# Optimization experiments

Hardware: AMD Instinct MI355X
Metric: run time of the kernel (lower is better)

The kernel has to match this reference:

```python
import jax, jax.numpy as jnp
import numpy as np

BS, N, D_IN, HID, D_OUT = 16, 256, 128, 128, 128


def setup_inputs() -> dict:
    key = jax.random.key(0)
    ks = jax.random.split(key, 10)
    s = 0.02
    return {
        "x": jax.random.normal(ks[0], (BS, N, D_IN), dtype=jnp.float32),
        "adj": jax.random.randint(ks[1], (BS, N, N), 0, 2, dtype=jnp.int32),
        "W_fc": jax.random.normal(ks[2], (D_IN, HID), dtype=jnp.float32) * s,
        "b_fc": jnp.zeros((HID,), dtype=jnp.float32),
        "W_a1": jax.random.normal(ks[3], (2 * HID, HID), dtype=jnp.float32) * s,
        "b_a1": jnp.zeros((HID,), dtype=jnp.float32),
        "w_a2": jax.random.normal(ks[4], (HID,), dtype=jnp.float32) * s,
        "b_a2": jnp.zeros((), dtype=jnp.float32),
        "W_out": jax.random.normal(ks[5], (HID, D_OUT), dtype=jnp.float32) * s,
        "b_out": jnp.zeros((D_OUT,), dtype=jnp.float32),
    }


def reference(x, adj, W_fc, b_fc, W_a1, b_a1, w_a2, b_a2, W_out, b_out):
    # h = fc(x): (bs, n, hid)
    h = jnp.einsum("bnd,dh->bnh", x, W_fc) + b_fc
    # attn first layer on concat([h_i, h_j]) decomposes into two half-projections
    # (same math as Linear(2*hid, hid) on the concatenated pair features).
    a_i = jnp.einsum("bnh,hk->bnk", h, W_a1[:HID])  # contribution of h_i
    a_j = jnp.einsum("bnh,hk->bnk", h, W_a1[HID:])  # contribution of h_j
    pre = a_i[:, :, None, :] + a_j[:, None, :, :] + b_a1  # (bs, n, n, hid)
    e = jnp.einsum("bijk,k->bij", jax.nn.relu(pre), w_a2) + b_a2  # (bs, n, n)
    e = jnp.where(adj == 0, jnp.float32(-1e9), e)
    attn = jax.nn.softmax(e, axis=-1)
    h_prime = jnp.einsum("bij,bjh->bih", attn, h)
    out = jnp.einsum("bih,ho->bio", h_prime, W_out) + b_out
    return out
```

## Files before the change

kernel.cpp:

```cpp
#include <hip/hip_runtime.h>

#define BS  16
#define NN  256
#define HID 128

__device__ __forceinline__ int xcd_swz(int bid) {
    return (bid & 7) * 64 + (bid >> 3);
}

__global__ __launch_bounds__(512, 4) void gat_k1(
    const float* __restrict__ x, const float* __restrict__ W_fc,
    const float* __restrict__ b_fc, const float* __restrict__ W_a1,
    const float* __restrict__ b_a1, const float* __restrict__ W_out,
    float* __restrict__ aiT, float* __restrict__ ajT, float* __restrict__ g)
{
    __shared__ __align__(16) float xs[8][HID];
    __shared__ __align__(16) float hs[8][HID];
    __shared__ __align__(16) float red[4][8][HID];

    const int tid = threadIdx.x;
    const int k   = tid & 127;
    const int q   = tid >> 7;
    const int swz = xcd_swz(blockIdx.x);
    const int r0  = swz * 8;
    const int b   = r0 >> 8;
    const int n0  = r0 & 255;

    for (int t = tid; t < 8 * HID; t += 512)
        xs[t >> 7][t & 127] = x[r0 * HID + t];
    __syncthreads();

    {
        float acc[8] = {0,0,0,0,0,0,0,0};
        const int dq = 32 * q;
        #pragma unroll 2
        for (int d = 0; d < 32; d += 4) {
            float w[4];
            #pragma unroll
            for (int t = 0; t < 4; ++t) w[t] = W_fc[(dq + d + t) * HID + k];
            #pragma unroll
            for (int r = 0; r < 8; ++r) {
                const float4 xv = *(const float4*)&xs[r][dq + d];
                acc[r] += xv.x * w[0] + xv.y * w[1] + xv.z * w[2] + xv.w * w[3];
            }
        }
        #pragma unroll
        for (int r = 0; r < 8; ++r) red[q][r][k] = acc[r];
    }
    __syncthreads();

    {
        const float bf = b_fc[k];
        #pragma unroll
        for (int r2 = 0; r2 < 2; ++r2) {
            const int r = 2 * q + r2;
            hs[r][k] = (red[0][r][k] + red[1][r][k])
                     + (red[2][r][k] + red[3][r][k]) + bf;
        }
    }
    __syncthreads();

    {
        const int is_aj = q >> 1;
        const int half  = q & 1;
        const float* Wp = W_a1 + (is_aj * HID + half * 64) * HID;
        float acc[8] = {0,0,0,0,0,0,0,0};
        const int hb = half * 64;
        #pragma unroll 2
        for (int d = 0; d < 64; d += 4) {
            float w[4];
            #pragma unroll
            for (int t = 0; t < 4; ++t) w[t] = Wp[(d + t) * HID + k];
            #pragma unroll
            for (int r = 0; r < 8; ++r) {
                const float4 hv = *(const float4*)&hs[r][hb + d];
                acc[r] += hv.x * w[0] + hv.y * w[1] + hv.z * w[2] + hv.w * w[3];
            }
        }
        #pragma unroll
        for (int r = 0; r < 8; ++r) red[q][r][k] = acc[r];
    }
    __syncthreads();

    {
        const int is_aj = q >> 1;
        const int rb4   = (q & 1) * 4;
        const float bias = is_aj ? 0.f : b_a1[k];
        const int p0 = 2 * is_aj, p1 = 2 * is_aj + 1;
        float4 v;
        v.x = red[p0][rb4 + 0][k] + red[p1][rb4 + 0][k] + bias;
        v.y = red[p0][rb4 + 1][k] + red[p1][rb4 + 1][k] + bias;
        v.z = red[p0][rb4 + 2][k] + red[p1][rb4 + 2][k] + bias;
        v.w = red[p0][rb4 + 3][k] + red[p1][rb4 + 3][k] + bias;
        float* dst = (is_aj ? ajT : aiT) + (b * HID + k) * NN + n0 + rb4;
        *(float4*)dst = v;
    }
    __syncthreads();

    {
        float acc[8] = {0,0,0,0,0,0,0,0};
        const int dq = 32 * q;
        #pragma unroll 2
        for (int d = 0; d < 32; d += 4) {
            float w[4];
            #pragma unroll
            for (int t = 0; t < 4; ++t) w[t] = W_out[(dq + d + t) * HID + k];
            #pragma unroll
            for (int r = 0; r < 8; ++r) {
                const float4 hv = *(const float4*)&hs[r][dq + d];
                acc[r] += hv.x * w[0] + hv.y * w[1] + hv.z * w[2] + hv.w * w[3];
            }
        }
        #pragma unroll
        for (int r = 0; r < 8; ++r) red[q][r][k] = acc[r];
    }
    __syncthreads();

    {
        #pragma unroll
        for (int r2 = 0; r2 < 2; ++r2) {
            const int r = 2 * q + r2;
            g[(r0 + r) * HID + k] = (red[0][r][k] + red[1][r][k])
                                  + (red[2][r][k] + red[3][r][k]);
        }
    }
}

__global__ __launch_bounds__(512, 4) void gat_k2(
    const float* __restrict__ aiT, const float* __restrict__ ajT,
    const float* __restrict__ g,  const int* __restrict__ adj,
    const float* __restrict__ w_a2, const float* __restrict__ b_a2,
    const float* __restrict__ b_out, float* __restrict__ out)
{
    __shared__ __align__(16) float aiw[HID][8];
    __shared__ __align__(16) float w2s[HID];
    __shared__ __align__(16) float ep[8][NN];
    __shared__ __align__(16) float red[4][8][HID];

    const int tid = threadIdx.x;
    const int swz = xcd_swz(blockIdx.x);
    const int b   = swz >> 5;
    const int i0  = (swz & 31) * 8;
    const int wv  = tid >> 6, lane = tid & 63;

    for (int t = tid; t < HID * 8; t += 512) {
        const int kk = t >> 3, r = t & 7;
        aiw[kk][r] = aiT[(b * HID + kk) * NN + i0 + r];
    }
    if (tid < HID) w2s[tid] = w_a2[tid];
    __syncthreads();

    const int jj = 32 * wv + (lane & 31);
    const int rg = lane >> 5;
    {
        int am[4];
        #pragma unroll
        for (int r = 0; r < 4; ++r)
            am[r] = adj[(b * NN + i0 + 4 * rg + r) * NN + jj];

        const float* ajp = ajT + b * HID * NN + jj;
        float acc[4] = {0.f, 0.f, 0.f, 0.f};
        #pragma unroll 8
        for (int kk = 0; kk < HID; ++kk) {
            const float a   = ajp[kk * NN];
            const float4 f4 = *(const float4*)&aiw[kk][4 * rg];
            const float wk  = w2s[kk];
            acc[0] += fmaxf(f4.x + a, 0.f) * wk;
            acc[1] += fmaxf(f4.y + a, 0.f) * wk;
            acc[2] += fmaxf(f4.z + a, 0.f) * wk;
            acc[3] += fmaxf(f4.w + a, 0.f) * wk;
        }
        const float ba2 = b_a2[0];
        #pragma unroll
        for (int r = 0; r < 4; ++r)
            ep[4 * rg + r][jj] = am[r] ? acc[r] + ba2 : -1e9f;
    }
    __syncthreads();

    {
        float4 e4 = *(const float4*)&ep[wv][4 * lane];
        float m = fmaxf(fmaxf(e4.x, e4.y), fmaxf(e4.z, e4.w));
        #pragma unroll
        for (int off = 32; off; off >>= 1) m = fmaxf(m, __shfl_xor(m, off));
        const float p0 = __expf(e4.x - m), p1 = __expf(e4.y - m);
        const float p2 = __expf(e4.z - m), p3 = __expf(e4.w - m);
        float s = (p0 + p1) + (p2 + p3);
        #pragma unroll
        for (int off = 32; off; off >>= 1) s += __shfl_xor(s, off);
        const float inv = 1.f / s;
        const float4 pv = {p0 * inv, p1 * inv, p2 * inv, p3 * inv};
        *(float4*)&ep[wv][4 * lane] = pv;
    }
    __syncthreads();

    const int k = tid & 127, qh = tid >> 7;
    {
        float o[8] = {0,0,0,0,0,0,0,0};
        const float* gb = g + (b * NN + qh * 64) * HID + k;
        const int jb = qh * 64;
        #pragma unroll 2
        for (int jq = 0; jq < 64; jq += 4) {
            const float g0 = gb[(jq + 0) * HID];
            const float g1 = gb[(jq + 1) * HID];
            const float g2 = gb[(jq + 2) * HID];
            const float g3 = gb[(jq + 3) * HID];
            #pragma unroll
            for (int r = 0; r < 8; ++r) {
                const float4 pv = *(const float4*)&ep[r][jb + jq];
                o[r] += pv.x * g0 + pv.y * g1 + pv.z * g2 + pv.w * g3;
            }
        }
        #pragma unroll
        for (int r = 0; r < 8; ++r) red[qh][r][k] = o[r];
    }
    __syncthreads();

    {
        const float bo = b_out[k];
        #pragma unroll
        for (int r2 = 0; r2 < 2; ++r2) {
            const int r = 2 * qh + r2;
            out[(b * NN + i0 + r) * HID + k] =
                (red[0][r][k] + red[1][r][k]) +
                (red[2][r][k] + red[3][r][k]) + bo;
        }
    }
}

extern "C" void kernel_launch(void* const* d_in, const int* in_sizes, int n_in,
                              void* d_out, int out_size, void* d_ws, size_t ws_size,
                              hipStream_t stream) {
    const float* x     = (const float*)d_in[0];
    const int*   adj   = (const int*)  d_in[1];
    const float* W_fc  = (const float*)d_in[2];
    const float* b_fc  = (const float*)d_in[3];
    const float* W_a1  = (const float*)d_in[4];
    const float* b_a1  = (const float*)d_in[5];
    const float* w_a2  = (const float*)d_in[6];
    const float* b_a2  = (const float*)d_in[7];
    const float* W_out = (const float*)d_in[8];
    const float* b_out = (const float*)d_in[9];
    float* out = (float*)d_out;

    float* ws  = (float*)d_ws;
    float* aiT = ws;
    float* ajT = ws + BS * NN * HID;
    float* g   = ws + 2 * BS * NN * HID;

    gat_k1<<<BS * NN / 8, 512, 0, stream>>>(x, W_fc, b_fc, W_a1, b_a1, W_out,
                                            aiT, ajT, g);
    gat_k2<<<BS * (NN / 8), 512, 0, stream>>>(aiT, ajT, g, adj, w_a2, b_a2,
                                              b_out, out);
}
```

Before: 41.41 us.

## Restructure attention score loop with split-K, register prefetch and uniform ai loads

The attention-score stage of the second kernel is reorganised. Each wave now handles 8 query rows by 64 key columns over half of the hidden dimension, instead of 4 rows by 32 columns over all of it. The ai values are read as wave-uniform float8 loads straight from global memory rather than staged through LDS. The aj values are double-buffered in registers, 16 at a time. The two hidden-dimension halves are summed through a shared buffer during softmax, the adjacency read becomes one int4 per lane, and several GEMM loops in both kernels are unrolled further. The aim is more independent work per thread and fewer LDS round trips, at the cost of higher register pressure and an extra partial-sum reduction.

```diff
diff --git a/kernel.cpp b/kernel.cpp
--- a/kernel.cpp
+++ b/kernel.cpp
@@ -3,6 +3,8 @@
 #define BS  16
 #define NN  256
 #define HID 128
+
+typedef __attribute__((ext_vector_type(8))) float float8;
 
 __device__ __forceinline__ int xcd_swz(int bid) {
     return (bid & 7) * 64 + (bid >> 3);
@@ -33,7 +35,7 @@
     {
         float acc[8] = {0,0,0,0,0,0,0,0};
         const int dq = 32 * q;
-        #pragma unroll 2
+        #pragma unroll 4
         for (int d = 0; d < 32; d += 4) {
             float w[4];
             #pragma unroll
@@ -66,7 +68,7 @@
         const float* Wp = W_a1 + (is_aj * HID + half * 64) * HID;
         float acc[8] = {0,0,0,0,0,0,0,0};
         const int hb = half * 64;
-        #pragma unroll 2
+        #pragma unroll 4
         for (int d = 0; d < 64; d += 4) {
             float w[4];
             #pragma unroll
@@ -100,7 +102,7 @@
     {
         float acc[8] = {0,0,0,0,0,0,0,0};
         const int dq = 32 * q;
-        #pragma unroll 2
+        #pragma unroll 4
         for (int d = 0; d < 32; d += 4) {
             float w[4];
             #pragma unroll
@@ -132,10 +134,8 @@
     const float* __restrict__ w_a2, const float* __restrict__ b_a2,
     const float* __restrict__ b_out, float* __restrict__ out)
 {
-    __shared__ __align__(16) float aiw[HID][8];
-    __shared__ __align__(16) float w2s[HID];
-    __shared__ __align__(16) float ep[8][NN];
-    __shared__ __align__(16) float red[4][8][HID];
+    __shared__ __align__(16) float buf[2 * 8 * NN];
+    __shared__ __align__(16) float ep[8 * NN];
 
     const int tid = threadIdx.x;
     const int swz = xcd_swz(blockIdx.x);
@@ -143,53 +143,79 @@
     const int i0  = (swz & 31) * 8;
     const int wv  = tid >> 6, lane = tid & 63;
 
-    for (int t = tid; t < HID * 8; t += 512) {
-        const int kk = t >> 3, r = t & 7;
-        aiw[kk][r] = aiT[(b * HID + kk) * NN + i0 + r];
-    }
-    if (tid < HID) w2s[tid] = w_a2[tid];
-    __syncthreads();
-
-    const int jj = 32 * wv + (lane & 31);
-    const int rg = lane >> 5;
-    {
-        int am[4];
-        #pragma unroll
-        for (int r = 0; r < 4; ++r)
-            am[r] = adj[(b * NN + i0 + 4 * rg + r) * NN + jj];
-
-        const float* ajp = ajT + b * HID * NN + jj;
-        float acc[4] = {0.f, 0.f, 0.f, 0.f};
-        #pragma unroll 8
-        for (int kk = 0; kk < HID; ++kk) {
-            const float a   = ajp[kk * NN];
-            const float4 f4 = *(const float4*)&aiw[kk][4 * rg];
-            const float wk  = w2s[kk];
-            acc[0] += fmaxf(f4.x + a, 0.f) * wk;
-            acc[1] += fmaxf(f4.y + a, 0.f) * wk;
-            acc[2] += fmaxf(f4.z + a, 0.f) * wk;
-            acc[3] += fmaxf(f4.w + a, 0.f) * wk;
-        }
+    const int4 am = *(const int4*)(adj + (b * NN + i0 + wv) * NN + 4 * lane);
+
+    const int kh = wv >> 2, jq = wv & 3;
+    const int j  = jq * 64 + lane;
+    {
+        const float* ajp = ajT + (b * HID + kh * 64) * NN + j;
+        const int aoff = __builtin_amdgcn_readfirstlane((b * HID + kh * 64) * NN + i0);
+        const float* aip = aiT + aoff;
+        const float* w2p = w_a2 + kh * 64;
+
+        float acc[8] = {0,0,0,0,0,0,0,0};
+        float pa[16], pb[16];
+        #pragma unroll
+        for (int t = 0; t < 16; ++t) pa[t] = ajp[t * NN];
+        #pragma unroll
+        for (int t = 0; t < 16; ++t) pb[t] = ajp[(16 + t) * NN];
+
+        #pragma unroll
+        for (int c = 0; c < 64; c += 32) {
+            #pragma unroll
+            for (int t = 0; t < 16; ++t) {
+                const int kk = c + t;
+                const float8 s8 = *(const float8*)(aip + kk * NN);
+                const float wk  = w2p[kk];
+                const float a   = pa[t];
+                #pragma unroll
+                for (int r = 0; r < 8; ++r)
+                    acc[r] += fmaxf(s8[r] + a, 0.f) * wk;
+            }
+            if (c + 32 < 64) {
+                #pragma unroll
+                for (int t = 0; t < 16; ++t) pa[t] = ajp[(c + 32 + t) * NN];
+            }
+            #pragma unroll
+            for (int t = 0; t < 16; ++t) {
+                const int kk = c + 16 + t;
+                const float8 s8 = *(const float8*)(aip + kk * NN);
+                const float wk  = w2p[kk];
+                const float a   = pb[t];
+                #pragma unroll
+                for (int r = 0; r < 8; ++r)
+                    acc[r] += fmaxf(s8[r] + a, 0.f) * wk;
+            }
+            if (c + 48 < 64) {
+                #pragma unroll
+                for (int t = 0; t < 16; ++t) pb[t] = ajp[(c + 48 + t) * NN];
+            }
+        }
+        #pragma unroll
+        for (int r = 0; r < 8; ++r)
+            buf[(kh * 8 + r) * NN + j] = acc[r];
+    }
+    __syncthreads();
+
+    {
         const float ba2 = b_a2[0];
-        #pragma unroll
-        for (int r = 0; r < 4; ++r)
-            ep[4 * rg + r][jj] = am[r] ? acc[r] + ba2 : -1e9f;
-    }
-    __syncthreads();
-
-    {
-        float4 e4 = *(const float4*)&ep[wv][4 * lane];
-        float m = fmaxf(fmaxf(e4.x, e4.y), fmaxf(e4.z, e4.w));
+        const float4 u = *(const float4*)&buf[(0 + wv) * NN + 4 * lane];
+        const float4 v = *(const float4*)&buf[(8 + wv) * NN + 4 * lane];
+        const float e0 = am.x ? u.x + v.x + ba2 : -1e9f;
+        const float e1 = am.y ? u.y + v.y + ba2 : -1e9f;
+        const float e2 = am.z ? u.z + v.z + ba2 : -1e9f;
+        const float e3 = am.w ? u.w + v.w + ba2 : -1e9f;
+        float m = fmaxf(fmaxf(e0, e1), fmaxf(e2, e3));
         #pragma unroll
         for (int off = 32; off; off >>= 1) m = fmaxf(m, __shfl_xor(m, off));
-        const float p0 = __expf(e4.x - m), p1 = __expf(e4.y - m);
-        const float p2 = __expf(e4.z - m), p3 = __expf(e4.w - m);
+        const float p0 = __expf(e0 - m), p1 = __expf(e1 - m);
+        const float p2 = __expf(e2 - m), p3 = __expf(e3 - m);
         float s = (p0 + p1) + (p2 + p3);
         #pragma unroll
         for (int off = 32; off; off >>= 1) s += __shfl_xor(s, off);
         const float inv = 1.f / s;
         const float4 pv = {p0 * inv, p1 * inv, p2 * inv, p3 * inv};
-        *(float4*)&ep[wv][4 * lane] = pv;
+        *(float4*)&ep[wv * NN + 4 * lane] = pv;
     }
     __syncthreads();
 
@@ -198,20 +224,20 @@
         float o[8] = {0,0,0,0,0,0,0,0};
         const float* gb = g + (b * NN + qh * 64) * HID + k;
         const int jb = qh * 64;
-        #pragma unroll 2
-        for (int jq = 0; jq < 64; jq += 4) {
-            const float g0 = gb[(jq + 0) * HID];
-            const float g1 = gb[(jq + 1) * HID];
-            const float g2 = gb[(jq + 2) * HID];
-            const float g3 = gb[(jq + 3) * HID];
-            #pragma unroll
-            for (int r = 0; r < 8; ++r) {
-                const float4 pv = *(const float4*)&ep[r][jb + jq];
+        #pragma unroll 4
+        for (int jq2 = 0; jq2 < 64; jq2 += 4) {
+            const float g0 = gb[(jq2 + 0) * HID];
+            const float g1 = gb[(jq2 + 1) * HID];
+            const float g2 = gb[(jq2 + 2) * HID];
+            const float g3 = gb[(jq2 + 3) * HID];
+            #pragma unroll
+            for (int r = 0; r < 8; ++r) {
+                const float4 pv = *(const float4*)&ep[r * NN + jb + jq2];
                 o[r] += pv.x * g0 + pv.y * g1 + pv.z * g2 + pv.w * g3;
             }
         }
         #pragma unroll
-        for (int r = 0; r < 8; ++r) red[qh][r][k] = o[r];
+        for (int r = 0; r < 8; ++r) buf[(qh * 8 + r) * HID + k] = o[r];
     }
     __syncthreads();
 
@@ -221,8 +247,8 @@
         for (int r2 = 0; r2 < 2; ++r2) {
             const int r = 2 * qh + r2;
             out[(b * NN + i0 + r) * HID + k] =
-                (red[0][r][k] + red[1][r][k]) +
-                (red[2][r][k] + red[3][r][k]) + bo;
+                (buf[(0 + r) * HID + k]  + buf[(8 + r) * HID + k]) +
+                (buf[(16 + r) * HID + k] + buf[(24 + r) * HID + k]) + bo;
         }
     }
 }
```

Measured after the change: 44.08 us. 1.06x slower.

## Restructure attention score loop with relu identity and split-K across waves

Applied to the files above, without the earlier changes.

The edge-score loop in the second kernel uses relu(a+b) = max(a,-b) + b, which lets the a_j*w term sit in a shared accumulator while each term becomes a max and an FMA. Each wave now handles half of the hidden dimension and two rows over four columns per lane, using float4 loads of ajT. Partial sums go through a shared buffer and are combined in the softmax step, which also loads adj as int4. This aims to cut per-element ALU work and improve load vectorization, at the cost of an extra shared-memory reduction and sync, with the buffer reused as the later reduction scratch.

```diff
diff --git a/kernel.cpp b/kernel.cpp
--- a/kernel.cpp
+++ b/kernel.cpp
@@ -134,8 +134,8 @@
 {
     __shared__ __align__(16) float aiw[HID][8];
     __shared__ __align__(16) float w2s[HID];
+    __shared__ __align__(16) float buf[2][8][NN];
     __shared__ __align__(16) float ep[8][NN];
-    __shared__ __align__(16) float red[4][8][HID];
 
     const int tid = threadIdx.x;
     const int swz = xcd_swz(blockIdx.x);
@@ -148,42 +148,55 @@
         aiw[kk][r] = aiT[(b * HID + kk) * NN + i0 + r];
     }
     if (tid < HID) w2s[tid] = w_a2[tid];
-    __syncthreads();
-
-    const int jj = 32 * wv + (lane & 31);
-    const int rg = lane >> 5;
-    {
-        int am[4];
-        #pragma unroll
-        for (int r = 0; r < 4; ++r)
-            am[r] = adj[(b * NN + i0 + 4 * rg + r) * NN + jj];
-
-        const float* ajp = ajT + b * HID * NN + jj;
-        float acc[4] = {0.f, 0.f, 0.f, 0.f};
+
+    const int4 am = *(const int4*)(adj + (b * NN + i0 + wv) * NN + 4 * lane);
+    __syncthreads();
+
+    const int kh = wv >> 2, rp = wv & 3;
+    {
+        const float* ajp = ajT + (b * HID + kh * 64) * NN + 4 * lane;
+        float4 acc0 = {0,0,0,0}, acc1 = {0,0,0,0}, saw = {0,0,0,0};
+        const int kb = kh * 64;
         #pragma unroll 8
-        for (int kk = 0; kk < HID; ++kk) {
-            const float a   = ajp[kk * NN];
-            const float4 f4 = *(const float4*)&aiw[kk][4 * rg];
-            const float wk  = w2s[kk];
-            acc[0] += fmaxf(f4.x + a, 0.f) * wk;
-            acc[1] += fmaxf(f4.y + a, 0.f) * wk;
-            acc[2] += fmaxf(f4.z + a, 0.f) * wk;
-            acc[3] += fmaxf(f4.w + a, 0.f) * wk;
-        }
+        for (int t = 0; t < 64; ++t) {
+            const float4 a4 = *(const float4*)(ajp + t * NN);
+            const float2 f2 = *(const float2*)&aiw[kb + t][2 * rp];
+            const float wk  = w2s[kb + t];
+            saw.x  = __builtin_fmaf(a4.x, wk, saw.x);
+            saw.y  = __builtin_fmaf(a4.y, wk, saw.y);
+            saw.z  = __builtin_fmaf(a4.z, wk, saw.z);
+            saw.w  = __builtin_fmaf(a4.w, wk, saw.w);
+            acc0.x = __builtin_fmaf(fmaxf(f2.x, -a4.x), wk, acc0.x);
+            acc0.y = __builtin_fmaf(fmaxf(f2.x, -a4.y), wk, acc0.y);
+            acc0.z = __builtin_fmaf(fmaxf(f2.x, -a4.z), wk, acc0.z);
+            acc0.w = __builtin_fmaf(fmaxf(f2.x, -a4.w), wk, acc0.w);
+            acc1.x = __builtin_fmaf(fmaxf(f2.y, -a4.x), wk, acc1.x);
+            acc1.y = __builtin_fmaf(fmaxf(f2.y, -a4.y), wk, acc1.y);
+            acc1.z = __builtin_fmaf(fmaxf(f2.y, -a4.z), wk, acc1.z);
+            acc1.w = __builtin_fmaf(fmaxf(f2.y, -a4.w), wk, acc1.w);
+        }
+        const float4 e0 = {acc0.x + saw.x, acc0.y + saw.y,
+                           acc0.z + saw.z, acc0.w + saw.w};
+        const float4 e1 = {acc1.x + saw.x, acc1.y + saw.y,
+                           acc1.z + saw.z, acc1.w + saw.w};
+        *(float4*)&buf[kh][2 * rp + 0][4 * lane] = e0;
+        *(float4*)&buf[kh][2 * rp + 1][4 * lane] = e1;
+    }
+    __syncthreads();
+
+    {
         const float ba2 = b_a2[0];
-        #pragma unroll
-        for (int r = 0; r < 4; ++r)
-            ep[4 * rg + r][jj] = am[r] ? acc[r] + ba2 : -1e9f;
-    }
-    __syncthreads();
-
-    {
-        float4 e4 = *(const float4*)&ep[wv][4 * lane];
-        float m = fmaxf(fmaxf(e4.x, e4.y), fmaxf(e4.z, e4.w));
+        const float4 u = *(const float4*)&buf[0][wv][4 * lane];
+        const float4 v = *(const float4*)&buf[1][wv][4 * lane];
+        const float e0 = am.x ? u.x + v.x + ba2 : -1e9f;
+        const float e1 = am.y ? u.y + v.y + ba2 : -1e9f;
+        const float e2 = am.z ? u.z + v.z + ba2 : -1e9f;
+        const float e3 = am.w ? u.w + v.w + ba2 : -1e9f;
+        float m = fmaxf(fmaxf(e0, e1), fmaxf(e2, e3));
         #pragma unroll
         for (int off = 32; off; off >>= 1) m = fmaxf(m, __shfl_xor(m, off));
-        const float p0 = __expf(e4.x - m), p1 = __expf(e4.y - m);
-        const float p2 = __expf(e4.z - m), p3 = __expf(e4.w - m);
+        const float p0 = __expf(e0 - m), p1 = __expf(e1 - m);
+        const float p2 = __expf(e2 - m), p3 = __expf(e3 - m);
         float s = (p0 + p1) + (p2 + p3);
         #pragma unroll
         for (int off = 32; off; off >>= 1) s += __shfl_xor(s, off);
@@ -193,6 +206,7 @@
     }
     __syncthreads();
 
+    float* red = &buf[0][0][0];
     const int k = tid & 127, qh = tid >> 7;
     {
         float o[8] = {0,0,0,0,0,0,0,0};
@@ -211,7 +225,7 @@
             }
         }
         #pragma unroll
-        for (int r = 0; r < 8; ++r) red[qh][r][k] = o[r];
+        for (int r = 0; r < 8; ++r) red[(qh * 8 + r) * HID + k] = o[r];
     }
     __syncthreads();
 
@@ -221,8 +235,8 @@
         for (int r2 = 0; r2 < 2; ++r2) {
             const int r = 2 * qh + r2;
             out[(b * NN + i0 + r) * HID + k] =
-                (red[0][r][k] + red[1][r][k]) +
-                (red[2][r][k] + red[3][r][k]) + bo;
+                (red[(0 + r) * HID + k]  + red[(8 + r) * HID + k]) +
+                (red[(16 + r) * HID + k] + red[(24 + r) * HID + k]) + bo;
         }
     }
 }
```

Result: no change. 41.54 us (+0.3%).

## Rewrite GAT attention-score loop with relu identity and split-K waves, enlarge fc tile

Applied to the files above, without the earlier changes.

The attention-score kernel now uses relu(a+b) = max(a,-b) + b. The per-j term sum(aj*w) is accumulated once per column instead of per row pair. Each wave handles a quarter of the hidden dimension over half the columns, for all 8 rows, and the partial sums are reduced through shared memory. Adjacency is loaded as int4, and the final attn@g stage splits j across waves with float2 loads and an 8-way shared reduction. The projection kernel processes 16 rows per block instead of 8, which halves the grid to 256 blocks to reuse weight loads but raises register and LDS use per block.

```diff
diff --git a/kernel.cpp b/kernel.cpp
--- a/kernel.cpp
+++ b/kernel.cpp
@@ -4,7 +4,10 @@
 #define NN  256
 #define HID 128
 
-__device__ __forceinline__ int xcd_swz(int bid) {
+__device__ __forceinline__ int xcd_swz256(int bid) {
+    return (bid & 7) * 32 + (bid >> 3);
+}
+__device__ __forceinline__ int xcd_swz512(int bid) {
     return (bid & 7) * 64 + (bid >> 3);
 }
 
@@ -14,24 +17,26 @@
     const float* __restrict__ b_a1, const float* __restrict__ W_out,
     float* __restrict__ aiT, float* __restrict__ ajT, float* __restrict__ g)
 {
-    __shared__ __align__(16) float xs[8][HID];
-    __shared__ __align__(16) float hs[8][HID];
-    __shared__ __align__(16) float red[4][8][HID];
+    __shared__ __align__(16) float xs[16][HID];
+    __shared__ __align__(16) float hs[16][HID];
+    __shared__ __align__(16) float red[4][16][HID];
 
     const int tid = threadIdx.x;
     const int k   = tid & 127;
     const int q   = tid >> 7;
-    const int swz = xcd_swz(blockIdx.x);
-    const int r0  = swz * 8;
+    const int swz = xcd_swz256(blockIdx.x);
+    const int r0  = swz * 16;
     const int b   = r0 >> 8;
     const int n0  = r0 & 255;
 
-    for (int t = tid; t < 8 * HID; t += 512)
+    for (int t = tid; t < 16 * HID; t += 512)
         xs[t >> 7][t & 127] = x[r0 * HID + t];
     __syncthreads();
 
     {
-        float acc[8] = {0,0,0,0,0,0,0,0};
+        float acc[16];
+        #pragma unroll
+        for (int r = 0; r < 16; ++r) acc[r] = 0.f;
         const int dq = 32 * q;
         #pragma unroll 2
         for (int d = 0; d < 32; d += 4) {
@@ -39,21 +44,21 @@
             #pragma unroll
             for (int t = 0; t < 4; ++t) w[t] = W_fc[(dq + d + t) * HID + k];
             #pragma unroll
-            for (int r = 0; r < 8; ++r) {
+            for (int r = 0; r < 16; ++r) {
                 const float4 xv = *(const float4*)&xs[r][dq + d];
                 acc[r] += xv.x * w[0] + xv.y * w[1] + xv.z * w[2] + xv.w * w[3];
             }
         }
         #pragma unroll
-        for (int r = 0; r < 8; ++r) red[q][r][k] = acc[r];
+        for (int r = 0; r < 16; ++r) red[q][r][k] = acc[r];
     }
     __syncthreads();
 
     {
         const float bf = b_fc[k];
         #pragma unroll
-        for (int r2 = 0; r2 < 2; ++r2) {
-            const int r = 2 * q + r2;
+        for (int r2 = 0; r2 < 4; ++r2) {
+            const int r = 4 * q + r2;
             hs[r][k] = (red[0][r][k] + red[1][r][k])
                      + (red[2][r][k] + red[3][r][k]) + bf;
         }
@@ -64,7 +69,9 @@
         const int is_aj = q >> 1;
         const int half  = q & 1;
         const float* Wp = W_a1 + (is_aj * HID + half * 64) * HID;
-        float acc[8] = {0,0,0,0,0,0,0,0};
+        float acc[16];
+        #pragma unroll
+        for (int r = 0; r < 16; ++r) acc[r] = 0.f;
         const int hb = half * 64;
         #pragma unroll 2
         for (int d = 0; d < 64; d += 4) {
@@ -72,33 +79,35 @@
             #pragma unroll
             for (int t = 0; t < 4; ++t) w[t] = Wp[(d + t) * HID + k];
             #pragma unroll
-            for (int r = 0; r < 8; ++r) {
+            for (int r = 0; r < 16; ++r) {
                 const float4 hv = *(const float4*)&hs[r][hb + d];
                 acc[r] += hv.x * w[0] + hv.y * w[1] + hv.z * w[2] + hv.w * w[3];
             }
         }
         #pragma unroll
-        for (int r = 0; r < 8; ++r) red[q][r][k] = acc[r];
+        for (int r = 0; r < 16; ++r) red[q][r][k] = acc[r];
     }
     __syncthreads();
 
     {
         const int is_aj = q >> 1;
-        const int rb4   = (q & 1) * 4;
+        const int rb8   = (q & 1) * 8;
         const float bias = is_aj ? 0.f : b_a1[k];
         const int p0 = 2 * is_aj, p1 = 2 * is_aj + 1;
-        float4 v;
-        v.x = red[p0][rb4 + 0][k] + red[p1][rb4 + 0][k] + bias;
-        v.y = red[p0][rb4 + 1][k] + red[p1][rb4 + 1][k] + bias;
-        v.z = red[p0][rb4 + 2][k] + red[p1][rb4 + 2][k] + bias;
-        v.w = red[p0][rb4 + 3][k] + red[p1][rb4 + 3][k] + bias;
-        float* dst = (is_aj ? ajT : aiT) + (b * HID + k) * NN + n0 + rb4;
-        *(float4*)dst = v;
-    }
-    __syncthreads();
-
-    {
-        float acc[8] = {0,0,0,0,0,0,0,0};
+        float v[8];
+        #pragma unroll
+        for (int t = 0; t < 8; ++t)
+            v[t] = red[p0][rb8 + t][k] + red[p1][rb8 + t][k] + bias;
+        float* dst = (is_aj ? ajT : aiT) + (b * HID + k) * NN + n0 + rb8;
+        *(float4*)(dst + 0) = *(float4*)&v[0];
+        *(float4*)(dst + 4) = *(float4*)&v[4];
+    }
+    __syncthreads();
+
+    {
+        float acc[16];
+        #pragma unroll
+        for (int r = 0; r < 16; ++r) acc[r] = 0.f;
         const int dq = 32 * q;
         #pragma unroll 2
         for (int d = 0; d < 32; d += 4) {
@@ -106,20 +115,20 @@
             #pragma unroll
             for (int t = 0; t < 4; ++t) w[t] = W_out[(dq + d + t) * HID + k];
             #pragma unroll
-            for (int r = 0; r < 8; ++r) {
+            for (int r = 0; r < 16; ++r) {
                 const float4 hv = *(const float4*)&hs[r][dq + d];
                 acc[r] += hv.x * w[0] + hv.y * w[1] + hv.z * w[2] + hv.w * w[3];
             }
         }
         #pragma unroll
-        for (int r = 0; r < 8; ++r) red[q][r][k] = acc[r];
-    }
-    __syncthreads();
-
-    {
-        #pragma unroll
-        for (int r2 = 0; r2 < 2; ++r2) {
-            const int r = 2 * q + r2;
+        for (int r = 0; r < 16; ++r) red[q][r][k] = acc[r];
+    }
+    __syncthreads();
+
+    {
+        #pragma unroll
+        for (int r2 = 0; r2 < 4; ++r2) {
+            const int r = 4 * q + r2;
             g[(r0 + r) * HID + k] = (red[0][r][k] + red[1][r][k])
                                   + (red[2][r][k] + red[3][r][k]);
         }
@@ -132,58 +141,84 @@
     const float* __restrict__ w_a2, const float* __restrict__ b_a2,
     const float* __restrict__ b_out, float* __restrict__ out)
 {
-    __shared__ __align__(16) float aiw[HID][8];
-    __shared__ __align__(16) float w2s[HID];
-    __shared__ __align__(16) float ep[8][NN];
-    __shared__ __align__(16) float red[4][8][HID];
+    __shared__ __align__(16) float4 aiwp[HID][2];
+    __shared__ __align__(16) float  w2s[HID];
+    __shared__ __align__(16) float  buf4[4][8][NN];
+    __shared__ __align__(16) float  ep[8][NN];
 
     const int tid = threadIdx.x;
-    const int swz = xcd_swz(blockIdx.x);
+    const int swz = xcd_swz512(blockIdx.x);
     const int b   = swz >> 5;
     const int i0  = (swz & 31) * 8;
     const int wv  = tid >> 6, lane = tid & 63;
 
-    for (int t = tid; t < HID * 8; t += 512) {
-        const int kk = t >> 3, r = t & 7;
-        aiw[kk][r] = aiT[(b * HID + kk) * NN + i0 + r];
-    }
-    if (tid < HID) w2s[tid] = w_a2[tid];
-    __syncthreads();
-
-    const int jj = 32 * wv + (lane & 31);
-    const int rg = lane >> 5;
-    {
-        int am[4];
-        #pragma unroll
-        for (int r = 0; r < 4; ++r)
-            am[r] = adj[(b * NN + i0 + 4 * rg + r) * NN + jj];
-
-        const float* ajp = ajT + b * HID * NN + jj;
-        float acc[4] = {0.f, 0.f, 0.f, 0.f};
+    if (tid < 256) {
+        const int kk = tid >> 1, rh = tid & 1;
+        aiwp[kk][rh] = *(const float4*)&aiT[(b * HID + kk) * NN + i0 + 4 * rh];
+    } else if (tid < 384) {
+        w2s[tid - 256] = w_a2[tid - 256];
+    }
+    const int4 am = *(const int4*)(adj + (b * NN + i0 + wv) * NN + 4 * lane);
+    __syncthreads();
+
+    {
+        const int kh = wv >> 1, jh = wv & 1;
+        const int kb = kh * 32, jb = jh * 128;
+        const float* ajp = ajT + (b * HID + kb) * NN + jb + 2 * lane;
+        float2 acc[8];
+        #pragma unroll
+        for (int r = 0; r < 8; ++r) { acc[r].x = 0.f; acc[r].y = 0.f; }
+        float2 saw = {0.f, 0.f};
         #pragma unroll 8
-        for (int kk = 0; kk < HID; ++kk) {
-            const float a   = ajp[kk * NN];
-            const float4 f4 = *(const float4*)&aiw[kk][4 * rg];
-            const float wk  = w2s[kk];
-            acc[0] += fmaxf(f4.x + a, 0.f) * wk;
-            acc[1] += fmaxf(f4.y + a, 0.f) * wk;
-            acc[2] += fmaxf(f4.z + a, 0.f) * wk;
-            acc[3] += fmaxf(f4.w + a, 0.f) * wk;
-        }
+        for (int t = 0; t < 32; ++t) {
+            const float2 a2 = *(const float2*)(ajp + t * NN);
+            const float4 aw0 = aiwp[kb + t][0];
+            const float4 aw1 = aiwp[kb + t][1];
+            const float wk   = w2s[kb + t];
+            saw.x = __builtin_fmaf(a2.x, wk, saw.x);
+            saw.y = __builtin_fmaf(a2.y, wk, saw.y);
+            acc[0].x = __builtin_fmaf(fmaxf(aw0.x, -a2.x), wk, acc[0].x);
+            acc[0].y = __builtin_fmaf(fmaxf(aw0.x, -a2.y), wk, acc[0].y);
+            acc[1].x = __builtin_fmaf(fmaxf(aw0.y, -a2.x), wk, acc[1].x);
+            acc[1].y = __builtin_fmaf(fmaxf(aw0.y, -a2.y), wk, acc[1].y);
+            acc[2].x = __builtin_fmaf(fmaxf(aw0.z, -a2.x), wk, acc[2].x);
+            acc[2].y = __builtin_fmaf(fmaxf(aw0.z, -a2.y), wk, acc[2].y);
+            acc[3].x = __builtin_fmaf(fmaxf(aw0.w, -a2.x), wk, acc[3].x);
+            acc[3].y = __builtin_fmaf(fmaxf(aw0.w, -a2.y), wk, acc[3].y);
+            acc[4].x = __builtin_fmaf(fmaxf(aw1.x, -a2.x), wk, acc[4].x);
+            acc[4].y = __builtin_fmaf(fmaxf(aw1.x, -a2.y), wk, acc[4].y);
+            acc[5].x = __builtin_fmaf(fmaxf(aw1.y, -a2.x), wk, acc[5].x);
+            acc[5].y = __builtin_fmaf(fmaxf(aw1.y, -a2.y), wk, acc[5].y);
+            acc[6].x = __builtin_fmaf(fmaxf(aw1.z, -a2.x), wk, acc[6].x);
+            acc[6].y = __builtin_fmaf(fmaxf(aw1.z, -a2.y), wk, acc[6].y);
+            acc[7].x = __builtin_fmaf(fmaxf(aw1.w, -a2.x), wk, acc[7].x);
+            acc[7].y = __builtin_fmaf(fmaxf(aw1.w, -a2.y), wk, acc[7].y);
+        }
+        #pragma unroll
+        for (int r = 0; r < 8; ++r) {
+            float2 e;
+            e.x = acc[r].x + saw.x;
+            e.y = acc[r].y + saw.y;
+            *(float2*)&buf4[kh][r][jb + 2 * lane] = e;
+        }
+    }
+    __syncthreads();
+
+    {
         const float ba2 = b_a2[0];
-        #pragma unroll
-        for (int r = 0; r < 4; ++r)
-            ep[4 * rg + r][jj] = am[r] ? acc[r] + ba2 : -1e9f;
-    }
-    __syncthreads();
-
-    {
-        float4 e4 = *(const float4*)&ep[wv][4 * lane];
-        float m = fmaxf(fmaxf(e4.x, e4.y), fmaxf(e4.z, e4.w));
+        const float4 s0 = *(const float4*)&buf4[0][wv][4 * lane];
+        const float4 s1 = *(const float4*)&buf4[1][wv][4 * lane];
+        const float4 s2 = *(const float4*)&buf4[2][wv][4 * lane];
+        const float4 s3 = *(const float4*)&buf4[3][wv][4 * lane];
+        const float e0 = am.x ? (s0.x + s1.x) + (s2.x + s3.x) + ba2 : -1e9f;
+        const float e1 = am.y ? (s0.y + s1.y) + (s2.y + s3.y) + ba2 : -1e9f;
+        const float e2 = am.z ? (s0.z + s1.z) + (s2.z + s3.z) + ba2 : -1e9f;
+        const float e3 = am.w ? (s0.w + s1.w) + (s2.w + s3.w) + ba2 : -1e9f;
+        float m = fmaxf(fmaxf(e0, e1), fmaxf(e2, e3));
         #pragma unroll
         for (int off = 32; off; off >>= 1) m = fmaxf(m, __shfl_xor(m, off));
-        const float p0 = __expf(e4.x - m), p1 = __expf(e4.y - m);
-        const float p2 = __expf(e4.z - m), p3 = __expf(e4.w - m);
+        const float p0 = __expf(e0 - m), p1 = __expf(e1 - m);
+        const float p2 = __expf(e2 - m), p3 = __expf(e3 - m);
         float s = (p0 + p1) + (p2 + p3);
         #pragma unroll
         for (int off = 32; off; off >>= 1) s += __shfl_xor(s, off);
@@ -193,36 +228,43 @@
     }
     __syncthreads();
 
-    const int k = tid & 127, qh = tid >> 7;
-    {
-        float o[8] = {0,0,0,0,0,0,0,0};
-        const float* gb = g + (b * NN + qh * 64) * HID + k;
-        const int jb = qh * 64;
-        #pragma unroll 2
-        for (int jq = 0; jq < 64; jq += 4) {
-            const float g0 = gb[(jq + 0) * HID];
-            const float g1 = gb[(jq + 1) * HID];
-            const float g2 = gb[(jq + 2) * HID];
-            const float g3 = gb[(jq + 3) * HID];
+    float* red = &buf4[0][0][0];
+    {
+        float2 o[8];
+        #pragma unroll
+        for (int r = 0; r < 8; ++r) { o[r].x = 0.f; o[r].y = 0.f; }
+        const int jb = 32 * wv;
+        const float* gb = g + (b * NN + jb) * HID + 2 * lane;
+        #pragma unroll 2
+        for (int jq = 0; jq < 32; jq += 4) {
+            const float2 g0 = *(const float2*)(gb + (jq + 0) * HID);
+            const float2 g1 = *(const float2*)(gb + (jq + 1) * HID);
+            const float2 g2 = *(const float2*)(gb + (jq + 2) * HID);
+            const float2 g3 = *(const float2*)(gb + (jq + 3) * HID);
             #pragma unroll
             for (int r = 0; r < 8; ++r) {
                 const float4 pv = *(const float4*)&ep[r][jb + jq];
-                o[r] += pv.x * g0 + pv.y * g1 + pv.z * g2 + pv.w * g3;
-            }
-        }
-        #pragma unroll
-        for (int r = 0; r < 8; ++r) red[qh][r][k] = o[r];
-    }
-    __syncthreads();
-
-    {
+                o[r].x += pv.x * g0.x + pv.y * g1.x + pv.z * g2.x + pv.w * g3.x;
+                o[r].y += pv.x * g0.y + pv.y * g1.y + pv.z * g2.y + pv.w * g3.y;
+            }
+        }
+        #pragma unroll
+        for (int r = 0; r < 8; ++r)
+            *(float2*)&red[(wv * 8 + r) * HID + 2 * lane] = o[r];
+    }
+    __syncthreads();
+
+    {
+        const int k = tid & 127, q = tid >> 7;
         const float bo = b_out[k];
         #pragma unroll
         for (int r2 = 0; r2 < 2; ++r2) {
-            const int r = 2 * qh + r2;
-            out[(b * NN + i0 + r) * HID + k] =
-                (red[0][r][k] + red[1][r][k]) +
-                (red[2][r][k] + red[3][r][k]) + bo;
+            const int r = 2 * q + r2;
+            float s = 0.f;
+            #pragma unroll
+            for (int oct = 0; oct < 8; ++oct)
+                s += red[(oct * 8 + r) * HID + k];
+            out[(b * NN + i0 + r) * HID + k] = s + bo;
         }
     }
 }
@@ -247,8 +289,8 @@
     float* ajT = ws + BS * NN * HID;
     float* g   = ws + 2 * BS * NN * HID;
 
-    gat_k1<<<BS * NN / 8, 512, 0, stream>>>(x, W_fc, b_fc, W_a1, b_a1, W_out,
-                                            aiT, ajT, g);
+    gat_k1<<<BS * NN / 16, 512, 0, stream>>>(x, W_fc, b_fc, W_a1, b_a1, W_out,
+                                             aiT, ajT, g);
     gat_k2<<<BS * (NN / 8), 512, 0, stream>>>(aiT, ajT, g, adj, w_a2, b_a2,
                                               b_out, out);
 }
```

Result: slower. 42.70 us (+3.1%).
